# Kernel tuning notes

Hardware: AMD Instinct MI355X
Metric: run time of the kernel (lower is better)

The kernel has to match this reference:

```python
import jax, jax.numpy as jnp
import numpy as np

D_MODEL = 1024
N_HEADS = 16
D_FF = 4096
ROPE_THETA = 10000.0


def _rope(x, pos):
    # x: [B, H, S, D], pos: [S]
    D = x.shape[-1]
    inv_freq = ROPE_THETA ** (-jnp.arange(0, D, 2, dtype=jnp.float32) / D)  # [D/2]
    ang = pos.astype(jnp.float32)[:, None] * inv_freq[None, :]              # [S, D/2]
    cos, sin = jnp.cos(ang), jnp.sin(ang)
    x1, x2 = x[..., 0::2], x[..., 1::2]
    r1 = x1 * cos - x2 * sin
    r2 = x1 * sin + x2 * cos
    return jnp.stack([r1, r2], axis=-1).reshape(x.shape)


def _rmsnorm(x, g, eps=1e-5):
    xf = x.astype(jnp.float32)
    rms = jnp.sqrt(jnp.mean(xf * xf, axis=-1, keepdims=True) + eps)
    return (xf / rms * g).astype(x.dtype)


def _block(x, WQ, WK, WV, WO, W1, W2, W3, G1, G2):
    B, S, _ = x.shape
    H, Dh = N_HEADS, D_MODEL // N_HEADS
    pos = jnp.arange(S)

    h = _rmsnorm(x, G1)
    Q = (h @ WQ.T).reshape(B, S, H, Dh).transpose(0, 2, 1, 3)
    K = (h @ WK.T).reshape(B, S, H, Dh).transpose(0, 2, 1, 3)
    V = (h @ WV.T).reshape(B, S, H, Dh).transpose(0, 2, 1, 3)
    Q = _rope(Q, pos)
    K = _rope(K, pos)

    scores = jnp.einsum('bhqd,bhkd->bhqk', Q, K) / jnp.sqrt(jnp.float32(Dh))
    causal = jnp.triu(jnp.ones((S, S), dtype=bool), k=1)
    scores = jnp.where(causal, -jnp.inf, scores.astype(jnp.float32))
    probs = jax.nn.softmax(scores, axis=-1).astype(x.dtype)
    attn = jnp.einsum('bhqk,bhkd->bhqd', probs, V)
    attn = attn.transpose(0, 2, 1, 3).reshape(B, S, D_MODEL)
    x = x + attn @ WO.T

    h = _rmsnorm(x, G2)
    w1x = h @ W1.T
    w3x = h @ W3.T
    ffn = (w1x * jax.nn.sigmoid(w1x) * w3x) @ W2.T
    return x + ffn


def setup_inputs() -> dict:
    key = jax.random.key(0)
    ks = jax.random.split(key, 9)
    sig_a = np.sqrt(2.0 / (D_MODEL + D_MODEL))
    sig_f = np.sqrt(2.0 / (D_FF + D_MODEL))
    x = jax.random.normal(ks[0], (2, 2048, D_MODEL), dtype=jnp.float32)
    def tn(k, shape, sig):
        return jnp.clip(jax.random.normal(k, shape, dtype=jnp.float32) * sig, -3 * sig, 3 * sig)
    return {
        'x': x,
        'WQ': tn(ks[1], (D_MODEL, D_MODEL), sig_a),
        'WK': tn(ks[2], (D_MODEL, D_MODEL), sig_a),
        'WV': tn(ks[3], (D_MODEL, D_MODEL), sig_a),
        'WO': tn(ks[4], (D_MODEL, D_MODEL), sig_a),
        'W1': tn(ks[5], (D_FF, D_MODEL), sig_f),
        'W2': tn(ks[6], (D_MODEL, D_FF), sig_f),
        'W3': tn(ks[7], (D_FF, D_MODEL), sig_f),
        'G1': jnp.ones((D_MODEL,), dtype=jnp.float32),
        'G2': jnp.ones((D_MODEL,), dtype=jnp.float32),
    }


def reference(x, WQ, WK, WV, WO, W1, W2, W3, G1, G2):
    return _block(x, WQ, WK, WV, WO, W1, W2, W3, G1, G2)
```

## Files before the change

### kernel.cpp

```cpp
#include <hip/hip_runtime.h>
#include <stdint.h>

typedef __attribute__((ext_vector_type(8))) short bf16x8;
typedef __attribute__((ext_vector_type(4))) short short4v;
typedef __attribute__((ext_vector_type(4))) float f32x4;

#define MFMA16(a, b, c) __builtin_amdgcn_mfma_f32_16x16x32_bf16((a), (b), (c), 0, 0, 0)

__device__ __forceinline__ float b2f(short s) {
  unsigned u = ((unsigned)(unsigned short)s) << 16;
  return __builtin_bit_cast(float, u);
}
__device__ __forceinline__ short f2b(float f) {
  unsigned u = __builtin_bit_cast(unsigned, f);
  u = (u + 0x7fffu + ((u >> 16) & 1u)) >> 16;
  return (short)u;
}

__device__ __forceinline__ void gl_lds16(const short* g, short* l) {
  __builtin_amdgcn_global_load_lds((const __attribute__((address_space(1))) void*)g,
                                   (__attribute__((address_space(3))) void*)l, 16, 0, 0);
}

__global__ __launch_bounds__(256) void convert_kernel(const float* __restrict__ src,
                                                      short* __restrict__ dst, int n) {
  int i = (blockIdx.x * 256 + threadIdx.x) * 8;
  if (i >= n) return;
  f32x4 a = *(const f32x4*)(src + i);
  f32x4 b = *(const f32x4*)(src + i + 4);
  short4v o0, o1;
#pragma unroll
  for (int j = 0; j < 4; ++j) { o0[j] = f2b(a[j]); o1[j] = f2b(b[j]); }
  *(short4v*)(dst + i) = o0;
  *(short4v*)(dst + i + 4) = o1;
}

__global__ __launch_bounds__(256) void rmsnorm_f32(const float* __restrict__ X,
                                                   const float* __restrict__ G,
                                                   short* __restrict__ O) {
  int row = blockIdx.x;
  int t = threadIdx.x;
  f32x4 v = *(const f32x4*)(X + (size_t)row * 1024 + t * 4);
  float ss = 0.f;
#pragma unroll
  for (int j = 0; j < 4; ++j) ss += v[j] * v[j];
#pragma unroll
  for (int d = 1; d < 64; d <<= 1) ss += __shfl_xor(ss, d, 64);
  __shared__ float red[4];
  if ((t & 63) == 0) red[t >> 6] = ss;
  __syncthreads();
  float tot = red[0] + red[1] + red[2] + red[3];
  float rinv = rsqrtf(tot * (1.0f / 1024.0f) + 1e-5f);
  f32x4 g = *(const f32x4*)(G + t * 4);
  short4v o;
#pragma unroll
  for (int j = 0; j < 4; ++j) o[j] = f2b(v[j] * rinv * g[j]);
  *(short4v*)(O + (size_t)row * 1024 + t * 4) = o;
}

template <int MODE>
__global__ __launch_bounds__(256) void gemm_bt(const short* __restrict__ A,
                                               const short* __restrict__ Bt,
                                               const void* Res, void* C,
                                               void* C1, void* C2,
                                               int M, int N, int K) {
  __shared__ __attribute__((aligned(16))) short Alds[2][128 * 32];
  __shared__ __attribute__((aligned(16))) short Blds[2][128 * 32];
  int tid = threadIdx.x;
  int lane = tid & 63, w = tid >> 6;
  int wr = w >> 1, wc = w & 1;
  int l15 = lane & 15, lg = lane >> 4;
  int m0 = blockIdx.y * 128, n0 = blockIdx.x * 128;
  void* Cw = C;
  int ncol0 = n0;
  int seg = 0;
  if (MODE == 3) {
    seg = n0 >> 10;
    Cw = (seg == 0) ? C : (seg == 1) ? C1 : C2;
    ncol0 = n0 & 1023;
  }
  f32x4 acc[4][4] = {};
  int arow = tid >> 2, acol = (tid & 3) * 8;
  const short* Ap = A + (size_t)(m0 + arow) * K + acol;
  const short* Bp = Bt + (size_t)(n0 + arow) * K + acol;
  int wb = w * 512;
#define STAGE_BT(buf, k0s)                                   \
  {                                                          \
    gl_lds16(Ap + (k0s), &Alds[buf][0] + wb);                \
    gl_lds16(Ap + (size_t)64 * K + (k0s), &Alds[buf][0] + 2048 + wb); \
    gl_lds16(Bp + (k0s), &Blds[buf][0] + wb);                \
    gl_lds16(Bp + (size_t)64 * K + (k0s), &Blds[buf][0] + 2048 + wb); \
  }
  STAGE_BT(0, 0);
  __syncthreads();
  int cur = 0;
  for (int k0 = 0; k0 < K; k0 += 32) {
    if (k0 + 32 < K) STAGE_BT(cur ^ 1, k0 + 32);
    bf16x8 af[4], bfr[4];
#pragma unroll
    for (int i = 0; i < 4; ++i) {
      af[i] = *(const bf16x8*)(&Alds[cur][0] + (wr * 64 + i * 16 + l15) * 32 + lg * 8);
      bfr[i] = *(const bf16x8*)(&Blds[cur][0] + (wc * 64 + i * 16 + l15) * 32 + lg * 8);
    }
#pragma unroll
    for (int mi = 0; mi < 4; ++mi)
#pragma unroll
      for (int ni = 0; ni < 4; ++ni)
        acc[mi][ni] = MFMA16(af[mi], bfr[ni], acc[mi][ni]);
    __syncthreads();
    cur ^= 1;
  }
#undef STAGE_BT
#pragma unroll
  for (int mi = 0; mi < 4; ++mi) {
#pragma unroll
    for (int r = 0; r < 4; ++r) {
      int row = m0 + wr * 64 + mi * 16 + lg * 4 + r;
      size_t base = (size_t)row * N;
#pragma unroll
      for (int ni = 0; ni < 4; ++ni) {
        int col = ncol0 + wc * 64 + ni * 16 + l15;
        float v = acc[mi][ni][r];
        if (MODE == 3 && seg <= 1) {
          int pos = row & 2047;
          int ii = (col & 62) >> 1;
          float invf2 = exp2f(-(float)ii * 0.4152410118f) * 0.15915494309f;
          float rev = (float)pos * invf2;
          rev -= rintf(rev);
          float angr = rev * 6.28318530718f;
          float sn = __sinf(angr), cs = __cosf(angr);
          float partner = __shfl_xor(v, 1, 64);
          float t = partner * sn;
          v = v * cs + (((l15 & 1) == 0) ? -t : t);
        }
        if (MODE == 2) {
          float rr = b2f(((const short*)Res)[base + col]);
          v = rr / (1.f + __expf(-rr)) * v;
          ((short*)Cw)[base + col] = f2b(v);
        } else {
          ((short*)Cw)[base + col] = f2b(v);
        }
      }
    }
  }
}

template <int MODE>
__global__ __launch_bounds__(512) void gemm256(const short* __restrict__ A,
                                               const short* __restrict__ Bt,
                                               const void* Res, void* C,
                                               int M, int N, int K) {
  __shared__ __attribute__((aligned(16))) short Alds[4][256 * 32];
  __shared__ __attribute__((aligned(16))) short Blds[4][256 * 32];
  int tid = threadIdx.x;
  int lane = tid & 63, w = tid >> 6;
  int wr = w >> 2, wc = w & 3;
  int l15 = lane & 15, lg = lane >> 4;
  int wg = blockIdx.x;
  int swz = (wg & 7) * 32 + (wg >> 3);
  int by = swz >> 4, bx = swz & 15;
  int m0 = by * 256, n0 = bx * 256;
  f32x4 acc[8][4] = {};
  int o0 = tid, o1 = 512 + tid;
  int r0 = o0 >> 2, cs0 = (o0 & 3) ^ ((r0 >> 1) & 3);
  int r1 = o1 >> 2, cs1 = (o1 & 3) ^ ((r1 >> 1) & 3);
  const short* Ap0 = A + (size_t)(m0 + r0) * K + cs0 * 8;
  const short* Ap1 = A + (size_t)(m0 + r1) * K + cs1 * 8;
  const short* Bp0 = Bt + (size_t)(n0 + r0) * K + cs0 * 8;
  const short* Bp1 = Bt + (size_t)(n0 + r1) * K + cs1 * 8;
  int wb = w * 512;
#define STAGE_256(buf, k0s)                              \
  {                                                      \
    gl_lds16(Ap0 + (k0s), &Alds[buf][0] + wb);           \
    gl_lds16(Ap1 + (k0s), &Alds[buf][0] + 4096 + wb);    \
    gl_lds16(Bp0 + (k0s), &Blds[buf][0] + wb);           \
    gl_lds16(Bp1 + (k0s), &Blds[buf][0] + 4096 + wb);    \
  }
  int nk = K >> 5;
  STAGE_256(0, 0);
  STAGE_256(1, 32);
  asm volatile("s_waitcnt vmcnt(4)" ::: "memory");
  __builtin_amdgcn_s_barrier();
  asm volatile("" ::: "memory");
  for (int kt = 0; kt < nk; ++kt) {
    int buf = kt & 3;
    if (kt + 2 < nk) STAGE_256((kt + 2) & 3, (kt + 2) * 32);
    bf16x8 af[8], bfr[4];
#pragma unroll
    for (int i = 0; i < 8; ++i) {
      int ra = wr * 128 + i * 16 + l15;
      int ua = lg ^ ((ra >> 1) & 3);
      af[i] = *(const bf16x8*)(&Alds[buf][0] + ra * 32 + ua * 8);
    }
#pragma unroll
    for (int n = 0; n < 4; ++n) {
      int rb = wc * 64 + n * 16 + l15;
      int ub = lg ^ ((rb >> 1) & 3);
      bfr[n] = *(const bf16x8*)(&Blds[buf][0] + rb * 32 + ub * 8);
    }
#pragma unroll
    for (int i = 0; i < 8; ++i)
#pragma unroll
      for (int n = 0; n < 4; ++n)
        acc[i][n] = MFMA16(af[i], bfr[n], acc[i][n]);
    if (kt + 2 < nk) {
      asm volatile("s_waitcnt vmcnt(4)" ::: "memory");
    } else {
      asm volatile("s_waitcnt vmcnt(0)" ::: "memory");
    }
    __builtin_amdgcn_s_barrier();
    asm volatile("" ::: "memory");
  }
#undef STAGE_256
#pragma unroll
  for (int i = 0; i < 8; ++i) {
#pragma unroll
    for (int r = 0; r < 4; ++r) {
      int row = m0 + wr * 128 + i * 16 + lg * 4 + r;
      size_t base = (size_t)row * N;
#pragma unroll
      for (int n = 0; n < 4; ++n) {
        int col = n0 + wc * 64 + n * 16 + l15;
        float v = acc[i][n][r];
        if (MODE == 2) {
          float rr = b2f(((const short*)Res)[base + col]);
          v = rr / (1.f + __expf(-rr)) * v;
        }
        ((short*)C)[base + col] = f2b(v);
      }
    }
  }
}

__global__ __launch_bounds__(512) void gemm_wide(const short* __restrict__ A,
                                                 const short* __restrict__ Bt,
                                                 const float* Res, float* C,
                                                 int M, int N, int K) {
  __shared__ __attribute__((aligned(16))) short Alds[4][128 * 64];
  __shared__ __attribute__((aligned(16))) short Blds[4][128 * 64];
  int tid = threadIdx.x;
  int lane = tid & 63, w = tid >> 6;
  int wr = w >> 2, wc = w & 3;
  int l15 = lane & 15, lg = lane >> 4;
  int m0 = blockIdx.y * 128, n0 = blockIdx.x * 128;
  f32x4 acc[4][2] = {};
  int o0 = tid, o1 = 512 + tid;
  int r0 = o0 >> 3, cs0 = (o0 & 7) ^ (r0 & 7);
  int r1 = o1 >> 3, cs1 = (o1 & 7) ^ (r1 & 7);
  const short* Ap0 = A + (size_t)(m0 + r0) * K + cs0 * 8;
  const short* Ap1 = A + (size_t)(m0 + r1) * K + cs1 * 8;
  const short* Bp0 = Bt + (size_t)(n0 + r0) * K + cs0 * 8;
  const short* Bp1 = Bt + (size_t)(n0 + r1) * K + cs1 * 8;
  int wb = w * 512;
#define STG_W(buf, k0s)                                  \
  {                                                      \
    gl_lds16(Ap0 + (k0s), &Alds[buf][0] + wb);           \
    gl_lds16(Ap1 + (k0s), &Alds[buf][0] + 4096 + wb);    \
    gl_lds16(Bp0 + (k0s), &Blds[buf][0] + wb);           \
    gl_lds16(Bp1 + (k0s), &Blds[buf][0] + 4096 + wb);    \
  }
  int nk = K >> 6;
  STG_W(0, 0);
  STG_W(1, 64);
  asm volatile("s_waitcnt vmcnt(4)" ::: "memory");
  __builtin_amdgcn_s_barrier();
  asm volatile("" ::: "memory");
  for (int kt = 0; kt < nk; ++kt) {
    int buf = kt & 3;
    if (kt + 2 < nk) STG_W((kt + 2) & 3, (kt + 2) * 64);
    bf16x8 af[4][2], bfr[2][2];
#pragma unroll
    for (int i = 0; i < 4; ++i) {
      int ra = wr * 64 + i * 16 + l15;
#pragma unroll
      for (int kk = 0; kk < 2; ++kk) {
        int ua = (kk * 4 + lg) ^ (ra & 7);
        af[i][kk] = *(const bf16x8*)(&Alds[buf][0] + ra * 64 + ua * 8);
      }
    }
#pragma unroll
    for (int i = 0; i < 2; ++i) {
      int rb = wc * 32 + i * 16 + l15;
#pragma unroll
      for (int kk = 0; kk < 2; ++kk) {
        int ub = (kk * 4 + lg) ^ (rb & 7);
        bfr[i][kk] = *(const bf16x8*)(&Blds[buf][0] + rb * 64 + ub * 8);
      }
    }
#pragma unroll
    for (int kk = 0; kk < 2; ++kk)
#pragma unroll
      for (int mi = 0; mi < 4; ++mi)
#pragma unroll
        for (int ni = 0; ni < 2; ++ni)
          acc[mi][ni] = MFMA16(af[mi][kk], bfr[ni][kk], acc[mi][ni]);
    if (kt + 2 < nk) {
      asm volatile("s_waitcnt vmcnt(4)" ::: "memory");
    } else {
      asm volatile("s_waitcnt vmcnt(0)" ::: "memory");
    }
    __builtin_amdgcn_s_barrier();
    asm volatile("" ::: "memory");
  }
#undef STG_W
#pragma unroll
  for (int mi = 0; mi < 4; ++mi) {
#pragma unroll
    for (int r = 0; r < 4; ++r) {
      int row = m0 + wr * 64 + mi * 16 + lg * 4 + r;
      size_t base = (size_t)row * N;
#pragma unroll
      for (int ni = 0; ni < 2; ++ni) {
        int col = n0 + wc * 32 + ni * 16 + l15;
        C[base + col] = acc[mi][ni][r] + Res[base + col];
      }
    }
  }
}

__global__ __launch_bounds__(256) void vtranspose(const short* __restrict__ V,
                                                  short* __restrict__ Vt) {
  __shared__ short T[64 * 72];
  int bh = blockIdx.y;
  int s0 = blockIdx.x * 64;
  int t = threadIdx.x;
  int r = t >> 2, cq = t & 3;
  const short* src = V + (size_t)((bh >> 4) * 2048 + s0 + r) * 1024 + (bh & 15) * 64 + cq * 16;
  *(int4*)(T + r * 72 + cq * 16) = *(const int4*)src;
  *(int4*)(T + r * 72 + cq * 16 + 8) = *(const int4*)(src + 8);
  __syncthreads();
  int d = t >> 2, sq = t & 3;
  short* dst = Vt + (size_t)bh * 131072 + (size_t)d * 2048 + s0 + sq * 16;
#pragma unroll
  for (int q = 0; q < 4; ++q) {
    short4v o;
#pragma unroll
    for (int j = 0; j < 4; ++j) o[j] = T[(sq * 16 + q * 4 + j) * 72 + d];
    *(short4v*)(dst + q * 4) = o;
  }
}

__global__ __launch_bounds__(256) void attn6(const short* __restrict__ Q,
                                             const short* __restrict__ K,
                                             const short* __restrict__ Vt,
                                             short* __restrict__ O) {
  __shared__ __attribute__((aligned(16))) short Klds[2][64 * 64];
  __shared__ __attribute__((aligned(16))) short Vlds[2][64 * 64];
  __shared__ __attribute__((aligned(16))) short Ptlds[4][64 * 20];
  int bx = blockIdx.x;
  int bh = bx & 31;
  int qt = 31 - (bx >> 5);
  int tid = threadIdx.x;
  int w = tid >> 6, lane = tid & 63;
  int l15 = lane & 15, lg = lane >> 4;
  int qbase = qt * 64 + w * 16;
  size_t rowbase = (size_t)(bh >> 4) * 2048 * 1024 + (size_t)(bh & 15) * 64;
  const short* vtb = Vt + (size_t)bh * 131072;
  const short* Kb0 = K + rowbase;
  bf16x8 qf[2];
  {
    const short* qp = Q + rowbase + (size_t)(qbase + l15) * 1024 + lg * 8;
    qf[0] = *(const bf16x8*)qp;
    qf[1] = *(const bf16x8*)(qp + 32);
  }
  bf16x8 ones;
#pragma unroll
  for (int j = 0; j < 8; ++j) ones[j] = (short)0x3F80;
  f32x4 oacc[4] = {};
  f32x4 lacc = {};
  int nchunk = qt + 1;
  short* pt = Ptlds[w];
  int i0 = w * 64 + lane;
  int r0 = i0 >> 3, c0 = i0 & 7, cs0 = c0 ^ (r0 & 7);
  int i1 = 256 + i0;
  int r1 = i1 >> 3, c1 = i1 & 7, cs1 = c1 ^ (r1 & 7);
#define STAGE_KV(buf, kt)                                                      \
  {                                                                            \
    int ks = (kt) * 64;                                                        \
    gl_lds16(Kb0 + (size_t)(ks + r0) * 1024 + cs0 * 8, &Klds[buf][0] + i0 * 8);\
    gl_lds16(Kb0 + (size_t)(ks + r1) * 1024 + cs1 * 8, &Klds[buf][0] + i1 * 8);\
    gl_lds16(vtb + (size_t)r0 * 2048 + ks + cs0 * 8, &Vlds[buf][0] + i0 * 8);  \
    gl_lds16(vtb + (size_t)r1 * 2048 + ks + cs1 * 8, &Vlds[buf][0] + i1 * 8);  \
  }
  STAGE_KV(0, 0);
  __syncthreads();
  int cur = 0;
  for (int kt = 0; kt < nchunk; ++kt) {
    if (kt + 1 < nchunk) STAGE_KV(cur ^ 1, kt + 1);
    int kstart = kt * 64;
    f32x4 s[4] = {};
#pragma unroll
    for (int g = 0; g < 4; ++g) {
      int krow = g * 16 + l15;
      bf16x8 k0 = *(const bf16x8*)(&Klds[cur][0] + krow * 64 + ((lg ^ (l15 & 7)) * 8));
      bf16x8 k1 = *(const bf16x8*)(&Klds[cur][0] + krow * 64 + (((4 + lg) ^ (l15 & 7)) * 8));
      s[g] = MFMA16(qf[0], k0, s[g]);
      s[g] = MFMA16(qf[1], k1, s[g]);
    }
#pragma unroll
    for (int g = 0; g < 4; ++g) {
      short4v pk;
#pragma unroll
      for (int r = 0; r < 4; ++r) {
        int qg = qbase + lg * 4 + r;
        int kg = kstart + g * 16 + l15;
        float v = __expf(s[g][r] * 0.125f - 24.f);
        pk[r] = f2b((kg > qg) ? 0.f : v);
      }
      *(short4v*)(pt + (g * 16 + l15) * 20 + lg * 4) = pk;
    }
    bf16x8 pa0, pa1;
#pragma unroll
    for (int j = 0; j < 8; ++j) {
      pa0[j] = pt[(lg * 8 + j) * 20 + l15];
      pa1[j] = pt[(32 + lg * 8 + j) * 20 + l15];
    }
#pragma unroll
    for (int t = 0; t < 4; ++t) {
      int drow = t * 16 + l15;
      bf16x8 vf0 = *(const bf16x8*)(&Vlds[cur][0] + drow * 64 + ((lg ^ (l15 & 7)) * 8));
      bf16x8 vf1 = *(const bf16x8*)(&Vlds[cur][0] + drow * 64 + (((4 + lg) ^ (l15 & 7)) * 8));
      oacc[t] = MFMA16(pa0, vf0, oacc[t]);
      oacc[t] = MFMA16(pa1, vf1, oacc[t]);
    }
    lacc = MFMA16(pa0, ones, lacc);
    lacc = MFMA16(pa1, ones, lacc);
    __syncthreads();
    cur ^= 1;
  }
#undef STAGE_KV
#pragma unroll
  for (int t = 0; t < 4; ++t) {
#pragma unroll
    for (int r = 0; r < 4; ++r) {
      int row = qbase + lg * 4 + r;
      float denom = fmaxf(lacc[r], 1e-30f);
      O[rowbase + (size_t)row * 1024 + t * 16 + l15] = f2b(oacc[t][r] / denom);
    }
  }
}

extern "C" void kernel_launch(void* const* d_in, const int* in_sizes, int n_in,
                              void* d_out, int out_size, void* d_ws, size_t ws_size,
                              hipStream_t stream) {
  const float* xf = (const float*)d_in[0];
  const float* G1f = (const float*)d_in[8];
  const float* G2f = (const float*)d_in[9];
  char* ws = (char*)d_ws;
  const size_t MB = 1048576;
  short* Wslot = (short*)(ws);
  short* WOb   = (short*)(ws);
  short* Wcat  = (short*)(ws + 8 * MB);
  short* Vt    = (short*)(ws + 8 * MB);
  short* h     = (short*)(ws + 16 * MB);
  short* Qb    = (short*)(ws + 24 * MB);
  short* Kb    = (short*)(ws + 32 * MB);
  short* Vb    = (short*)(ws + 40 * MB);
  short* att   = (short*)(ws + 48 * MB);
  short* w1x   = Qb;
  float* x1f   = (float*)d_out;
  float* outf  = (float*)d_out;

  dim3 blk(256);
  convert_kernel<<<512, blk, 0, stream>>>((const float*)d_in[1], Wcat, 1048576);
  convert_kernel<<<512, blk, 0, stream>>>((const float*)d_in[2], Wcat + 1048576, 1048576);
  convert_kernel<<<512, blk, 0, stream>>>((const float*)d_in[3], Wcat + 2097152, 1048576);
  convert_kernel<<<512, blk, 0, stream>>>((const float*)d_in[4], WOb, 1048576);

  rmsnorm_f32<<<4096, blk, 0, stream>>>(xf, G1f, h);
  dim3 gqkv(24, 32);
  gemm_bt<3><<<gqkv, blk, 0, stream>>>(h, Wcat, nullptr, Qb, Kb, Vb, 4096, 1024, 1024);
  dim3 gvt(32, 32);
  vtranspose<<<gvt, blk, 0, stream>>>(Vb, Vt);
  attn6<<<1024, blk, 0, stream>>>(Qb, Kb, Vt, att);
  dim3 g1(8, 32);
  gemm_wide<<<g1, dim3(512), 0, stream>>>(att, WOb, xf, x1f, 4096, 1024, 1024);
  rmsnorm_f32<<<4096, blk, 0, stream>>>(x1f, G2f, h);
  convert_kernel<<<2048, blk, 0, stream>>>((const float*)d_in[5], Wslot, 4194304);
  gemm256<0><<<256, dim3(512), 0, stream>>>(h, Wslot, nullptr, w1x, 4096, 4096, 1024);
  convert_kernel<<<2048, blk, 0, stream>>>((const float*)d_in[7], Wslot, 4194304);
  gemm256<2><<<256, dim3(512), 0, stream>>>(h, Wslot, w1x, w1x, 4096, 4096, 1024);
  convert_kernel<<<2048, blk, 0, stream>>>((const float*)d_in[6], Wslot, 4194304);
  gemm_wide<<<g1, dim3(512), 0, stream>>>(w1x, Wslot, x1f, outf, 4096, 1024, 4096);
}
```

Before: 346.8 us.

## Switch gemm256 to BK=64 double-buffered LDS pipeline with 8-way XOR swizzle

The gemm256 kernel moves from a 4-slot ring of 32-wide K tiles with prefetch distance two and manual vmcnt waits to two buffers of 64-wide K tiles. Each iteration issues the next tile's loads and then runs two 32-wide MFMA sub-steps before a full __syncthreads. This halves the number of barriers per K and widens the XOR swizzle to 8 chunks per row. In exchange the prefetch lead shrinks to one tile, and __syncthreads waits on all outstanding loads, which may expose global latency.

```diff
diff --git a/kernel.cpp b/kernel.cpp
--- a/kernel.cpp
+++ b/kernel.cpp
@@ -150,8 +150,8 @@
                                                const short* __restrict__ Bt,
                                                const void* Res, void* C,
                                                int M, int N, int K) {
-  __shared__ __attribute__((aligned(16))) short Alds[4][256 * 32];
-  __shared__ __attribute__((aligned(16))) short Blds[4][256 * 32];
+  __shared__ __attribute__((aligned(16))) short Alds[2][256 * 64];
+  __shared__ __attribute__((aligned(16))) short Blds[2][256 * 64];
   int tid = threadIdx.x;
   int lane = tid & 63, w = tid >> 6;
   int wr = w >> 2, wc = w & 3;
@@ -161,55 +161,48 @@
   int by = swz >> 4, bx = swz & 15;
   int m0 = by * 256, n0 = bx * 256;
   f32x4 acc[8][4] = {};
-  int o0 = tid, o1 = 512 + tid;
-  int r0 = o0 >> 2, cs0 = (o0 & 3) ^ ((r0 >> 1) & 3);
-  int r1 = o1 >> 2, cs1 = (o1 & 3) ^ ((r1 >> 1) & 3);
-  const short* Ap0 = A + (size_t)(m0 + r0) * K + cs0 * 8;
-  const short* Ap1 = A + (size_t)(m0 + r1) * K + cs1 * 8;
-  const short* Bp0 = Bt + (size_t)(n0 + r0) * K + cs0 * 8;
-  const short* Bp1 = Bt + (size_t)(n0 + r1) * K + cs1 * 8;
-  int wb = w * 512;
-#define STAGE_256(buf, k0s)                              \
-  {                                                      \
-    gl_lds16(Ap0 + (k0s), &Alds[buf][0] + wb);           \
-    gl_lds16(Ap1 + (k0s), &Alds[buf][0] + 4096 + wb);    \
-    gl_lds16(Bp0 + (k0s), &Blds[buf][0] + wb);           \
-    gl_lds16(Bp1 + (k0s), &Blds[buf][0] + 4096 + wb);    \
-  }
-  int nk = K >> 5;
+  int rr = tid >> 3;
+  int cs = (tid & 7) ^ (rr & 7);
+  const short* Apt = A + (size_t)(m0 + rr) * K + cs * 8;
+  const short* Bpt = Bt + (size_t)(n0 + rr) * K + cs * 8;
+#define STAGE_256(buf, kt)                                                     \
+  {                                                                            \
+    int ko = (kt) * 64;                                                        \
+    _Pragma("unroll")                                                          \
+    for (int j = 0; j < 4; ++j) {                                              \
+      gl_lds16(Apt + (size_t)(j * 64) * K + ko, &Alds[buf][0] + j * 4096 + w * 512); \
+      gl_lds16(Bpt + (size_t)(j * 64) * K + ko, &Blds[buf][0] + j * 4096 + w * 512); \
+    }                                                                          \
+  }
+  int nt = K >> 6;
   STAGE_256(0, 0);
-  STAGE_256(1, 32);
-  asm volatile("s_waitcnt vmcnt(4)" ::: "memory");
-  __builtin_amdgcn_s_barrier();
-  asm volatile("" ::: "memory");
-  for (int kt = 0; kt < nk; ++kt) {
-    int buf = kt & 3;
-    if (kt + 2 < nk) STAGE_256((kt + 2) & 3, (kt + 2) * 32);
-    bf16x8 af[8], bfr[4];
-#pragma unroll
-    for (int i = 0; i < 8; ++i) {
-      int ra = wr * 128 + i * 16 + l15;
-      int ua = lg ^ ((ra >> 1) & 3);
-      af[i] = *(const bf16x8*)(&Alds[buf][0] + ra * 32 + ua * 8);
-    }
-#pragma unroll
-    for (int n = 0; n < 4; ++n) {
-      int rb = wc * 64 + n * 16 + l15;
-      int ub = lg ^ ((rb >> 1) & 3);
-      bfr[n] = *(const bf16x8*)(&Blds[buf][0] + rb * 32 + ub * 8);
-    }
-#pragma unroll
-    for (int i = 0; i < 8; ++i)
-#pragma unroll
-      for (int n = 0; n < 4; ++n)
-        acc[i][n] = MFMA16(af[i], bfr[n], acc[i][n]);
-    if (kt + 2 < nk) {
-      asm volatile("s_waitcnt vmcnt(4)" ::: "memory");
-    } else {
-      asm volatile("s_waitcnt vmcnt(0)" ::: "memory");
-    }
-    __builtin_amdgcn_s_barrier();
-    asm volatile("" ::: "memory");
+  __syncthreads();
+  int cur = 0;
+  for (int kt = 0; kt < nt; ++kt) {
+    if (kt + 1 < nt) STAGE_256(cur ^ 1, kt + 1);
+#pragma unroll
+    for (int kk = 0; kk < 2; ++kk) {
+      bf16x8 af[8], bfr[4];
+#pragma unroll
+      for (int i = 0; i < 8; ++i) {
+        int ra = wr * 128 + i * 16 + l15;
+        int ua = (kk * 4 + lg) ^ (ra & 7);
+        af[i] = *(const bf16x8*)(&Alds[cur][0] + ra * 64 + ua * 8);
+      }
+#pragma unroll
+      for (int n = 0; n < 4; ++n) {
+        int rb = wc * 64 + n * 16 + l15;
+        int ub = (kk * 4 + lg) ^ (rb & 7);
+        bfr[n] = *(const bf16x8*)(&Blds[cur][0] + rb * 64 + ub * 8);
+      }
+#pragma unroll
+      for (int i = 0; i < 8; ++i)
+#pragma unroll
+        for (int n = 0; n < 4; ++n)
+          acc[i][n] = MFMA16(af[i], bfr[n], acc[i][n]);
+    }
+    __syncthreads();
+    cur ^= 1;
   }
 #undef STAGE_256
 #pragma unroll
@@ -223,8 +216,8 @@
         int col = n0 + wc * 64 + n * 16 + l15;
         float v = acc[i][n][r];
         if (MODE == 2) {
-          float rr = b2f(((const short*)Res)[base + col]);
-          v = rr / (1.f + __expf(-rr)) * v;
+          float rr2 = b2f(((const short*)Res)[base + col]);
+          v = rr2 / (1.f + __expf(-rr2)) * v;
         }
         ((short*)C)[base + col] = f2b(v);
       }
```

Measured after the change: 331.7 us. -4.4%, faster.
